# Kernel tuning notes

Measured on AMD Instinct MI355X. Metric: run time of the kernel, lower is better.

Reference implementation:

```python
import jax, jax.numpy as jnp
import numpy as np

B, S, D, H, E, K = 2, 1024, 768, 12, 8, 2
DF = 4 * D
HD = D // H
EPS = 1e-5

def layer_norm(x, g, b):
    m = jnp.mean(x, axis=-1, keepdims=True)
    v = jnp.mean(jnp.square(x - m), axis=-1, keepdims=True)
    return (x - m) * jax.lax.rsqrt(v + EPS) * g + b

def setup_inputs() -> dict:
    key = jax.random.key(0)
    ks = jax.random.split(key, 16)
    s = lambda i, shape, sc: jax.random.normal(ks[i], shape, jnp.float32) * sc
    return {
        'x': s(0, (B, S, D), 1.0),
        'ln1_g': jnp.ones((D,), jnp.float32), 'ln1_b': jnp.zeros((D,), jnp.float32),
        'Wq': s(1, (D, D), 0.02), 'Wk': s(2, (D, D), 0.02), 'Wv': s(3, (D, D), 0.02),
        'Wo': s(4, (D, D), 0.02), 'bo': jnp.zeros((D,), jnp.float32),
        'ln2_g': jnp.ones((D,), jnp.float32), 'ln2_b': jnp.zeros((D,), jnp.float32),
        'Wr': s(5, (D, E), 0.02), 'br': jnp.zeros((E,), jnp.float32),
        'W1': s(6, (E, D, DF), 0.02), 'b1': jnp.zeros((E, DF), jnp.float32),
        'W2': s(7, (E, DF, D), 0.02), 'b2': jnp.zeros((E, D), jnp.float32),
    }

def _attn(xn, Wq, Wk, Wv, Wo, bo):
    # xn: [B,S,D]
    q = (xn @ Wq).reshape(B, S, H, HD).transpose(0, 2, 1, 3)
    k = (xn @ Wk).reshape(B, S, H, HD).transpose(0, 2, 1, 3)
    v = (xn @ Wv).reshape(B, S, H, HD).transpose(0, 2, 1, 3)
    scores = jnp.einsum('bhqd,bhkd->bhqk', q, k) / jnp.sqrt(jnp.float32(HD))
    causal = jnp.tril(jnp.ones((S, S), bool))
    scores = jnp.where(causal, scores, jnp.float32(-1e9))
    w = jax.nn.softmax(scores, axis=-1)
    out = jnp.einsum('bhqk,bhkd->bhqd', w, v)
    out = out.transpose(0, 2, 1, 3).reshape(B, S, D)
    return out @ Wo + bo

def _smoe(xn, Wr, br, W1, b1, W2, b2):
    logits = xn @ Wr + br                               # [B,S,E]
    topv, topi = jax.lax.top_k(logits, K)               # [B,S,K]
    gw = jax.nn.softmax(topv, axis=-1)                  # softmax over selected experts
    oh = jax.nn.one_hot(topi, E, dtype=xn.dtype)        # [B,S,K,E]
    gate = jnp.einsum('bske,bsk->bse', oh, gw)          # sparse gate, zeros elsewhere
    h = jax.nn.gelu(jnp.einsum('bsd,edf->bsef', xn, W1) + b1, approximate=False)
    eo = jnp.einsum('bsef,efd->bsed', h, W2) + b2       # [B,S,E,D]
    return jnp.einsum('bsed,bse->bsd', eo, gate)

def reference(x, ln1_g, ln1_b, Wq, Wk, Wv, Wo, bo, ln2_g, ln2_b, Wr, br, W1, b1, W2, b2):
    h = x + _attn(layer_norm(x, ln1_g, ln1_b), Wq, Wk, Wv, Wo, bo)
    out = h + _smoe(layer_norm(h, ln2_g, ln2_b), Wr, br, W1, b1, W2, b2)
    return out
```

## Files before the change

kernel.cpp:

```cpp
#include <hip/hip_runtime.h>

using bf16x8 = __attribute__((ext_vector_type(8))) short;
using f32x4  = __attribute__((ext_vector_type(4))) float;

#define DEV __device__ __forceinline__

DEV short f2bf(float x){
  unsigned u = __float_as_uint(x);
  u += 0x7fffu + ((u >> 16) & 1u);
  return (short)(u >> 16);
}
DEV float bf2f(short h){ return __uint_as_float(((unsigned)(unsigned short)h) << 16); }

#define MFMA16(a,b,c) __builtin_amdgcn_mfma_f32_16x16x32_bf16(a,b,c,0,0,0)

DEV void gl_lds16(const void* g, void* l){
  __builtin_amdgcn_global_load_lds(
      (const __attribute__((address_space(1))) unsigned*)g,
      (__attribute__((address_space(3))) unsigned*)l, 16, 0, 0);
}


__global__ void k_transpose(const float* __restrict__ src, long sbatch,
                            short* __restrict__ dhi, short* __restrict__ dlo, long dbatch,
                            int R, int C){
  __shared__ float tile[64][65];
  const float* s = src + (long)blockIdx.z * sbatch;
  int c0 = blockIdx.x * 64, r0 = blockIdx.y * 64;
  int tx = threadIdx.x & 15, ty = threadIdx.x >> 4;
  #pragma unroll
  for (int i = 0; i < 4; i++){
    int r = ty + 16*i;
    float4 v = *(const float4*)&s[(long)(r0 + r) * C + c0 + tx*4];
    tile[r][tx*4+0] = v.x; tile[r][tx*4+1] = v.y;
    tile[r][tx*4+2] = v.z; tile[r][tx*4+3] = v.w;
  }
  __syncthreads();
  int rseg = (threadIdx.x & 7) * 8;
  #pragma unroll
  for (int p = 0; p < 2; p++){
    int col = (threadIdx.x >> 3) + 32*p;
    short hv[8], lv[8];
    #pragma unroll
    for (int k = 0; k < 8; k++){
      float v = tile[rseg + k][col];
      hv[k] = f2bf(v);
      lv[k] = f2bf(v - bf2f(hv[k]));
    }
    long o = (long)blockIdx.z * dbatch + (long)(c0 + col) * R + r0 + rseg;
    *(bf16x8*)&dhi[o] = *(bf16x8*)&hv[0];
    if (dlo) *(bf16x8*)&dlo[o] = *(bf16x8*)&lv[0];
  }
}

__global__ void k_ln1(const float* __restrict__ x, const float* __restrict__ g,
                      const float* __restrict__ bb,
                      short* __restrict__ xh, short* __restrict__ xl){
  int t = blockIdx.x, tid = threadIdx.x;
  const float* xr = x + (long)t * 768;
  float v[3];
  #pragma unroll
  for (int j = 0; j < 3; j++) v[j] = xr[tid + 256*j];
  float s = v[0]+v[1]+v[2];
  float q = v[0]*v[0]+v[1]*v[1]+v[2]*v[2];
  #pragma unroll
  for (int o = 32; o > 0; o >>= 1){ s += __shfl_down(s,o,64); q += __shfl_down(q,o,64); }
  __shared__ float ss[4], qs[4];
  int w = tid >> 6;
  if ((tid & 63) == 0){ ss[w] = s; qs[w] = q; }
  __syncthreads();
  float St = ss[0]+ss[1]+ss[2]+ss[3], Qt = qs[0]+qs[1]+qs[2]+qs[3];
  float mean = St * (1.f/768.f);
  float var  = Qt * (1.f/768.f) - mean*mean;
  float inv  = 1.f / sqrtf(var + 1e-5f);
  #pragma unroll
  for (int j = 0; j < 3; j++){
    int d = tid + 256*j;
    float xn = (v[j]-mean)*inv*g[d] + bb[d];
    short hv = f2bf(xn);
    xh[(long)t*768 + d] = hv;
    xl[(long)t*768 + d] = f2bf(xn - bf2f(hv));
  }
}

__global__ __launch_bounds__(256,2) void k_qkv(
    const short* __restrict__ Ah, const short* __restrict__ Al,
    const short* __restrict__ Bh, const short* __restrict__ Bl,
    short* __restrict__ qh, short* __restrict__ ql,
    short* __restrict__ kh, short* __restrict__ kl,
    short* __restrict__ vh, short* __restrict__ vl){
  int M0 = blockIdx.x * 128, N0 = blockIdx.y * 128;
  __shared__ __align__(16) short lah[128*64], lal[128*64], lbh[128*64], lbl[128*64];
  int tid = threadIdx.x;
  int w = tid >> 6, lane = tid & 63, l15 = lane & 15, quad = lane >> 4;
  int mbase = (w & 1) * 64, nbase = (w >> 1) * 64;
  f32x4 acc[4][4];
  #pragma unroll
  for (int i = 0; i < 4; i++)
    #pragma unroll
    for (int j = 0; j < 4; j++) acc[i][j] = (f32x4){0.f,0.f,0.f,0.f};
  int rl = lane >> 3, pch = lane & 7;
  long gA[4], gB[4];
  #pragma unroll
  for (int j = 0; j < 4; j++){
    int r = w*32 + j*8 + rl;
    int c = pch ^ (r & 7);
    gA[j] = (long)(M0 + r)*768 + c*8;
    gB[j] = (long)(N0 + r)*768 + c*8;
  }
  for (int k0 = 0; k0 < 768; k0 += 64){
    #pragma unroll
    for (int j = 0; j < 4; j++){
      gl_lds16(Ah + gA[j] + k0, lah + w*2048 + j*512);
      gl_lds16(Al + gA[j] + k0, lal + w*2048 + j*512);
      gl_lds16(Bh + gB[j] + k0, lbh + w*2048 + j*512);
      gl_lds16(Bl + gB[j] + k0, lbl + w*2048 + j*512);
    }
    __syncthreads();
    #pragma unroll
    for (int kk = 0; kk < 2; kk++){
      int swq = ((kk*4 + quad) ^ (l15 & 7)) * 8;
      bf16x8 afh[4], afl[4];
      #pragma unroll
      for (int mt = 0; mt < 4; mt++){
        afh[mt] = *(const bf16x8*)&lah[(mbase+mt*16+l15)*64 + swq];
        afl[mt] = *(const bf16x8*)&lal[(mbase+mt*16+l15)*64 + swq];
      }
      #pragma unroll
      for (int nt = 0; nt < 4; nt++){
        bf16x8 bfh = *(const bf16x8*)&lbh[(nbase+nt*16+l15)*64 + swq];
        bf16x8 bfl = *(const bf16x8*)&lbl[(nbase+nt*16+l15)*64 + swq];
        #pragma unroll
        for (int mt = 0; mt < 4; mt++){
          acc[mt][nt] = MFMA16(afh[mt], bfh, acc[mt][nt]);
          acc[mt][nt] = MFMA16(afh[mt], bfl, acc[mt][nt]);
          acc[mt][nt] = MFMA16(afl[mt], bfh, acc[mt][nt]);
        }
      }
    }
    __syncthreads();
  }
  #pragma unroll
  for (int mt = 0; mt < 4; mt++){
    #pragma unroll
    for (int nt = 0; nt < 4; nt++){
      #pragma unroll
      for (int rg = 0; rg < 4; rg++){
        int m = M0 + mbase + mt*16 + quad*4 + rg;
        int n = N0 + nbase + nt*16 + l15;
        float vv = acc[mt][nt][rg];
        int bi = m >> 10, si = m & 1023;
        if (n < 768){
          float sv = vv * 0.125f;
          short hv = f2bf(sv);
          int hh = n >> 6, hd = n & 63;
          long o = (((long)(bi*12+hh)*1024) + si)*64 + hd;
          qh[o] = hv; ql[o] = f2bf(sv - bf2f(hv));
        } else if (n < 1536){
          int n2 = n - 768;
          short hv = f2bf(vv);
          int hh = n2 >> 6, hd = n2 & 63;
          long o = (((long)(bi*12+hh)*1024) + si)*64 + hd;
          kh[o] = hv; kl[o] = f2bf(vv - bf2f(hv));
        } else {
          int n2 = n - 1536;
          short hv = f2bf(vv);
          int hh = n2 >> 6, hd = n2 & 63;
          long o = (((long)(bi*12+hh)*64) + hd)*1024 + si;
          vh[o] = hv; vl[o] = f2bf(vv - bf2f(hv));
        }
      }
    }
  }
}

__global__ __launch_bounds__(256,3) void k_attn(
    const short* __restrict__ qh, const short* __restrict__ ql,
    const short* __restrict__ kh, const short* __restrict__ kl,
    const short* __restrict__ vth, const short* __restrict__ vtl,
    float* __restrict__ po, float* __restrict__ pm, float* __restrict__ pl){
  int qt = blockIdx.x >> 1, half = blockIdx.x & 1, bh = blockIdx.y;
  int q0 = qt * 64;
  long base = (long)bh * 1024 * 64;
  int ktb = half ? ((qt + 2) >> 1) : 0;
  int kte = half ? (qt + 1) : ((qt + 2) >> 1);
  __shared__ __align__(16) short skh[64*64], skl[64*64], svh[64*64], svl[64*64];
  __shared__ __align__(16) short sph[4][16*72], spl[4][16*72];
  int tid = threadIdx.x, w = tid >> 6, lane = tid & 63, l15 = lane & 15, quad = lane >> 4;
  bf16x8 qfh[2], qfl[2];
  #pragma unroll
  for (int c = 0; c < 2; c++){
    long qa = base + (long)(q0 + w*16 + l15)*64 + c*32 + quad*8;
    qfh[c] = *(const bf16x8*)(qh + qa);
    qfl[c] = *(const bf16x8*)(ql + qa);
  }
  f32x4 oacc[4];
  #pragma unroll
  for (int i = 0; i < 4; i++) oacc[i] = (f32x4){0.f,0.f,0.f,0.f};
  float m_i[4] = {-1e30f,-1e30f,-1e30f,-1e30f};
  float l_i[4] = {0.f,0.f,0.f,0.f};
  const short* gsrc = (w==0) ? kh : (w==1) ? kl : (w==2) ? vth : vtl;
  short* myb = (w==0) ? skh : (w==1) ? skl : (w==2) ? svh : svl;
  bool isv = (w >= 2);
  int rloc = lane >> 3, pch = lane & 7;
  for (int kt = ktb; kt < kte; kt++){
    #pragma unroll
    for (int j = 0; j < 8; j++){
      int r = j*8 + rloc;
      int c = pch ^ (r & 7);
      long ga = isv ? (base + (long)r*1024 + kt*64 + c*8)
                    : (base + (long)(kt*64 + r)*64 + c*8);
      gl_lds16(gsrc + ga, myb + j*512);
    }
    __syncthreads();
    f32x4 sfr[4];
    #pragma unroll
    for (int nt = 0; nt < 4; nt++){
      f32x4 c = (f32x4){0.f,0.f,0.f,0.f};
      int krow = (nt*16 + l15) * 64;
      #pragma unroll
      for (int ch = 0; ch < 2; ch++){
        int pc = ((ch*4 + quad) ^ (l15 & 7)) * 8;
        bf16x8 kfh = *(const bf16x8*)&skh[krow + pc];
        bf16x8 kfl = *(const bf16x8*)&skl[krow + pc];
        c = MFMA16(qfh[ch], kfh, c);
        c = MFMA16(qfh[ch], kfl, c);
        c = MFMA16(qfl[ch], kfh, c);
      }
      sfr[nt] = c;
    }
    if (kt == qt){
      #pragma unroll
      for (int nt = 0; nt < 4; nt++)
        #pragma unroll
        for (int rg = 0; rg < 4; rg++){
          int kp = nt*16 + l15, qp = w*16 + quad*4 + rg;
          if (kp > qp) sfr[nt][rg] = -1e30f;
        }
    }
    float rmax[4];
    #pragma unroll
    for (int rg = 0; rg < 4; rg++)
      rmax[rg] = fmaxf(fmaxf(sfr[0][rg], sfr[1][rg]), fmaxf(sfr[2][rg], sfr[3][rg]));
    #pragma unroll
    for (int xm = 1; xm < 16; xm <<= 1)
      #pragma unroll
      for (int rg = 0; rg < 4; rg++)
        rmax[rg] = fmaxf(rmax[rg], __shfl_xor(rmax[rg], xm, 64));
    float alpha[4];
    #pragma unroll
    for (int rg = 0; rg < 4; rg++){
      float mn = fmaxf(m_i[rg], rmax[rg]);
      alpha[rg] = expf(m_i[rg] - mn);
      m_i[rg] = mn;
    }
    float rsum[4] = {0.f,0.f,0.f,0.f};
    #pragma unroll
    for (int nt = 0; nt < 4; nt++)
      #pragma unroll
      for (int rg = 0; rg < 4; rg++){
        float p = expf(sfr[nt][rg] - m_i[rg]);
        sfr[nt][rg] = p; rsum[rg] += p;
      }
    #pragma unroll
    for (int xm = 1; xm < 16; xm <<= 1)
      #pragma unroll
      for (int rg = 0; rg < 4; rg++)
        rsum[rg] += __shfl_xor(rsum[rg], xm, 64);
    #pragma unroll
    for (int rg = 0; rg < 4; rg++) l_i[rg] = l_i[rg]*alpha[rg] + rsum[rg];
    #pragma unroll
    for (int hd = 0; hd < 4; hd++)
      #pragma unroll
      for (int rg = 0; rg < 4; rg++) oacc[hd][rg] *= alpha[rg];
    #pragma unroll
    for (int nt = 0; nt < 4; nt++)
      #pragma unroll
      for (int rg = 0; rg < 4; rg++){
        float p = sfr[nt][rg];
        short hv = f2bf(p);
        sph[w][(quad*4+rg)*72 + nt*16 + l15] = hv;
        spl[w][(quad*4+rg)*72 + nt*16 + l15] = f2bf(p - bf2f(hv));
      }
    bf16x8 pfh[2], pfl[2];
    #pragma unroll
    for (int ch = 0; ch < 2; ch++){
      pfh[ch] = *(const bf16x8*)&sph[w][l15*72 + ch*32 + quad*8];
      pfl[ch] = *(const bf16x8*)&spl[w][l15*72 + ch*32 + quad*8];
    }
    #pragma unroll
    for (int hd = 0; hd < 4; hd++){
      int vrow = (hd*16 + l15) * 64;
      #pragma unroll
      for (int ch = 0; ch < 2; ch++){
        int pc = ((ch*4 + quad) ^ (l15 & 7)) * 8;
        bf16x8 vfh = *(const bf16x8*)&svh[vrow + pc];
        bf16x8 vfl = *(const bf16x8*)&svl[vrow + pc];
        oacc[hd] = MFMA16(pfh[ch], vfh, oacc[hd]);
        oacc[hd] = MFMA16(pfh[ch], vfl, oacc[hd]);
        oacc[hd] = MFMA16(pfl[ch], vfh, oacc[hd]);
      }
    }
    __syncthreads();
  }
  long pb = ((long)(half*24 + bh)*1024);
  #pragma unroll
  for (int hdt = 0; hdt < 4; hdt++)
    #pragma unroll
    for (int rg = 0; rg < 4; rg++){
      int qp = q0 + w*16 + quad*4 + rg;
      po[(pb + qp)*64 + hdt*16 + l15] = oacc[hdt][rg];
    }
  if (l15 == 0){
    #pragma unroll
    for (int rg = 0; rg < 4; rg++){
      int qp = q0 + w*16 + quad*4 + rg;
      pm[pb + qp] = m_i[rg];
      pl[pb + qp] = l_i[rg];
    }
  }
}

__global__ void k_attn_combine(const float* __restrict__ po, const float* __restrict__ pm,
                               const float* __restrict__ pl,
                               short* __restrict__ oh, short* __restrict__ ol){
  int bh = blockIdx.y, tid = threadIdx.x;
  int r = blockIdx.x*64 + (tid >> 2);
  int c0 = (tid & 3) * 16;
  long i0 = (long)bh*1024 + r;
  long i1 = (long)(24 + bh)*1024 + r;
  float m0 = pm[i0], m1 = pm[i1], l0 = pl[i0], l1 = pl[i1];
  float m = fmaxf(m0, m1);
  float a0 = expf(m0 - m), a1 = expf(m1 - m);
  float inv = 1.f / (a0*l0 + a1*l1);
  a0 *= inv; a1 *= inv;
  int b = bh / 12, hh = bh % 12;
  long ob = ((long)(b*1024 + r))*768 + hh*64 + c0;
  short hv[16], lv[16];
  #pragma unroll
  for (int j = 0; j < 4; j++){
    float4 o0 = *(const float4*)&po[i0*64 + c0 + j*4];
    float4 o1 = *(const float4*)&po[i1*64 + c0 + j*4];
    float vs[4] = {a0*o0.x + a1*o1.x, a0*o0.y + a1*o1.y,
                   a0*o0.z + a1*o1.z, a0*o0.w + a1*o1.w};
    #pragma unroll
    for (int q = 0; q < 4; q++){
      short h = f2bf(vs[q]);
      hv[j*4+q] = h; lv[j*4+q] = f2bf(vs[q] - bf2f(h));
    }
  }
  *(bf16x8*)(oh + ob)     = *(bf16x8*)&hv[0];
  *(bf16x8*)(oh + ob + 8) = *(bf16x8*)&hv[8];
  *(bf16x8*)(ol + ob)     = *(bf16x8*)&lv[0];
  *(bf16x8*)(ol + ob + 8) = *(bf16x8*)&lv[8];
}

__global__ __launch_bounds__(256,2) void k_wo(
    const short* __restrict__ Ah, const short* __restrict__ Al,
    const short* __restrict__ Bh, const short* __restrict__ Bl,
    const float* __restrict__ x, const float* __restrict__ bo,
    float* __restrict__ hout){
  int M0 = blockIdx.x * 128, N0 = blockIdx.y * 128;
  __shared__ __align__(16) short lah[128*64], lal[128*64], lbh[128*64], lbl[128*64];
  int tid = threadIdx.x;
  int w = tid >> 6, lane = tid & 63, l15 = lane & 15, quad = lane >> 4;
  int mbase = (w & 1) * 64, nbase = (w >> 1) * 64;
  f32x4 acc[4][4];
  #pragma unroll
  for (int i = 0; i < 4; i++)
    #pragma unroll
    for (int j = 0; j < 4; j++) acc[i][j] = (f32x4){0.f,0.f,0.f,0.f};
  int rl = lane >> 3, pch = lane & 7;
  long gA[4], gB[4];
  #pragma unroll
  for (int j = 0; j < 4; j++){
    int r = w*32 + j*8 + rl;
    int c = pch ^ (r & 7);
    gA[j] = (long)(M0 + r)*768 + c*8;
    gB[j] = (long)(N0 + r)*768 + c*8;
  }
  for (int k0 = 0; k0 < 768; k0 += 64){
    #pragma unroll
    for (int j = 0; j < 4; j++){
      gl_lds16(Ah + gA[j] + k0, lah + w*2048 + j*512);
      gl_lds16(Al + gA[j] + k0, lal + w*2048 + j*512);
      gl_lds16(Bh + gB[j] + k0, lbh + w*2048 + j*512);
      gl_lds16(Bl + gB[j] + k0, lbl + w*2048 + j*512);
    }
    __syncthreads();
    #pragma unroll
    for (int kk = 0; kk < 2; kk++){
      int swq = ((kk*4 + quad) ^ (l15 & 7)) * 8;
      bf16x8 afh[4], afl[4];
      #pragma unroll
      for (int mt = 0; mt < 4; mt++){
        afh[mt] = *(const bf16x8*)&lah[(mbase+mt*16+l15)*64 + swq];
        afl[mt] = *(const bf16x8*)&lal[(mbase+mt*16+l15)*64 + swq];
      }
      #pragma unroll
      for (int nt = 0; nt < 4; nt++){
        bf16x8 bfh = *(const bf16x8*)&lbh[(nbase+nt*16+l15)*64 + swq];
        bf16x8 bfl = *(const bf16x8*)&lbl[(nbase+nt*16+l15)*64 + swq];
        #pragma unroll
        for (int mt = 0; mt < 4; mt++){
          acc[mt][nt] = MFMA16(afh[mt], bfh, acc[mt][nt]);
          acc[mt][nt] = MFMA16(afh[mt], bfl, acc[mt][nt]);
          acc[mt][nt] = MFMA16(afl[mt], bfh, acc[mt][nt]);
        }
      }
    }
    __syncthreads();
  }
  #pragma unroll
  for (int mt = 0; mt < 4; mt++)
    #pragma unroll
    for (int nt = 0; nt < 4; nt++)
      #pragma unroll
      for (int rg = 0; rg < 4; rg++){
        int m = M0 + mbase + mt*16 + quad*4 + rg;
        int n = N0 + nbase + nt*16 + l15;
        hout[(long)m*768 + n] = acc[mt][nt][rg] + x[(long)m*768 + n] + bo[n];
      }
}

__global__ void k_ln2router(const float* __restrict__ h, const float* __restrict__ g,
                            const float* __restrict__ bb, const float* __restrict__ Wr,
                            const float* __restrict__ br, short* __restrict__ xn2,
                            int* __restrict__ sel, float* __restrict__ gw){
  int wv = (blockIdx.x*256 + threadIdx.x) >> 6;
  int lane = threadIdx.x & 63;
  #pragma unroll
  for (int rep = 0; rep < 2; rep++){
    int t = wv*2 + rep;
    const float* xr = h + (long)t * 768;
    float v[12];
    #pragma unroll
    for (int j = 0; j < 12; j++) v[j] = xr[lane + 64*j];
    float s = 0.f, q = 0.f;
    #pragma unroll
    for (int j = 0; j < 12; j++){ s += v[j]; q += v[j]*v[j]; }
    #pragma unroll
    for (int xm = 1; xm < 64; xm <<= 1){ s += __shfl_xor(s, xm, 64); q += __shfl_xor(q, xm, 64); }
    float mean = s * (1.f/768.f);
    float var  = q * (1.f/768.f) - mean*mean;
    float inv  = 1.f / sqrtf(var + 1e-5f);
    float part[8] = {0,0,0,0,0,0,0,0};
    #pragma unroll
    for (int j = 0; j < 12; j++){
      int d = lane + 64*j;
      float xn = (v[j]-mean)*inv*g[d] + bb[d];
      xn2[(long)t*768 + d] = f2bf(xn);
      #pragma unroll
      for (int e = 0; e < 8; e++) part[e] += xn * Wr[d*8 + e];
    }
    #pragma unroll
    for (int xm = 1; xm < 64; xm <<= 1)
      #pragma unroll
      for (int e = 0; e < 8; e++) part[e] += __shfl_xor(part[e], xm, 64);
    if (lane == 0){
      float lg[8];
      #pragma unroll
      for (int e = 0; e < 8; e++) lg[e] = part[e] + br[e];
      int i1 = 0;
      for (int e = 1; e < 8; e++) if (lg[e] > lg[i1]) i1 = e;
      int i2 = -1;
      for (int e = 0; e < 8; e++){ if (e == i1) continue; if (i2 < 0 || lg[e] > lg[i2]) i2 = e; }
      float e2 = expf(lg[i2] - lg[i1]);
      float is = 1.f / (1.f + e2);
      gw[t*2]   = is;
      gw[t*2+1] = e2 * is;
      sel[t*2]   = i1;
      sel[t*2+1] = i2;
    }
  }
}

__global__ void k_build(const int* __restrict__ sel, int* __restrict__ poffs,
                        int* __restrict__ mbc, int* __restrict__ ptot,
                        int* __restrict__ pperm, int* __restrict__ inv){
  __shared__ int cnt8[8], cur[8], wbase[16][8];
  int tid = threadIdx.x;
  int lane = tid & 63, wv = tid >> 6;
  if (tid < 8) cnt8[tid] = 0;
  __syncthreads();
  int sv[4];
  #pragma unroll
  for (int r = 0; r < 4; r++){
    sv[r] = sel[tid + r*1024];
    #pragma unroll
    for (int e = 0; e < 8; e++){
      unsigned long long mk = __ballot(sv[r] == e);
      if (lane == 0) atomicAdd(&cnt8[e], (int)__popcll(mk));
    }
  }
  __syncthreads();
  if (tid == 0){
    int p = 0;
    for (int e = 0; e < 8; e++){
      cur[e] = p; poffs[e] = p;
      int pc = (cnt8[e] + 127) & ~127;
      mbc[e] = pc >> 7;
      p += pc;
    }
    *ptot = p;
  }
  __syncthreads();
  #pragma unroll
  for (int r = 0; r < 5; r++) pperm[tid + r*1024] = -1;
  __syncthreads();
  unsigned long long lmask = (1ull << lane) - 1ull;
  #pragma unroll
  for (int r = 0; r < 4; r++){
    int s = sv[r];
    unsigned long long mk[8];
    #pragma unroll
    for (int e = 0; e < 8; e++) mk[e] = __ballot(s == e);
    if (lane == 0){
      #pragma unroll
      for (int e = 0; e < 8; e++)
        wbase[wv][e] = atomicAdd(&cur[e], (int)__popcll(mk[e]));
    }
    unsigned long long mks = 0;
    #pragma unroll
    for (int e = 0; e < 8; e++) if (s == e) mks = mk[e];
    int pos = wbase[wv][s] + (int)__popcll(mks & lmask);
    int i = tid + r*1024;
    pperm[pos] = i;
    inv[i] = pos;
  }
}

__global__ __launch_bounds__(256,3) void k_moe1(
    const short* __restrict__ xn2, const short* __restrict__ W1T,
    const float* __restrict__ b1,
    const int* __restrict__ poffs, const int* __restrict__ mbc,
    const int* __restrict__ pperm, short* __restrict__ h1){
  int t = blockIdx.x;
  int e = t / 24, n = t % 24;
  if ((int)blockIdx.y >= mbc[e]) return;
  int M0 = poffs[e] + blockIdx.y * 128;
  int N0 = n * 128;
  const short* Bp = W1T + (long)e * 3072 * 768;
  __shared__ __align__(16) short la[128*64], lb[128*64];
  __shared__ int rtok[128];
  int tid = threadIdx.x, w = tid >> 6, lane = tid & 63, l15 = lane & 15, quad = lane >> 4;
  if (tid < 128) rtok[tid] = pperm[M0 + tid];
  __syncthreads();
  int rl = lane >> 3, pch = lane & 7;
  long gA[4], gB[4];
  #pragma unroll
  for (int j = 0; j < 4; j++){
    int r = w*32 + j*8 + rl;
    int c = pch ^ (r & 7);
    int tk = rtok[r]; tk = (tk >= 0) ? (tk >> 1) : 0;
    gA[j] = (long)tk*768 + c*8;
    gB[j] = (long)(N0 + r)*768 + c*8;
  }
  short* ldA = la + w*2048;
  short* ldB = lb + w*2048;
  f32x4 acc[4][4];
  #pragma unroll
  for (int i = 0; i < 4; i++)
    #pragma unroll
    for (int j = 0; j < 4; j++) acc[i][j] = (f32x4){0.f,0.f,0.f,0.f};
  int mbase = (w & 1) * 64, nbase = (w >> 1) * 64;
  for (int k0 = 0; k0 < 768; k0 += 64){
    #pragma unroll
    for (int j = 0; j < 4; j++) gl_lds16(xn2 + gA[j] + k0, ldA + j*512);
    #pragma unroll
    for (int j = 0; j < 4; j++) gl_lds16(Bp  + gB[j] + k0, ldB + j*512);
    __syncthreads();
    #pragma unroll
    for (int kk = 0; kk < 2; kk++){
      int swq = ((kk*4 + quad) ^ (l15 & 7)) * 8;
      bf16x8 af[4];
      #pragma unroll
      for (int mt = 0; mt < 4; mt++)
        af[mt] = *(const bf16x8*)&la[(mbase+mt*16+l15)*64 + swq];
      #pragma unroll
      for (int nt = 0; nt < 4; nt++){
        bf16x8 bf = *(const bf16x8*)&lb[(nbase+nt*16+l15)*64 + swq];
        #pragma unroll
        for (int mt = 0; mt < 4; mt++) acc[mt][nt] = MFMA16(af[mt], bf, acc[mt][nt]);
      }
    }
    __syncthreads();
  }
  #pragma unroll
  for (int mt = 0; mt < 4; mt++)
    #pragma unroll
    for (int nt = 0; nt < 4; nt++)
      #pragma unroll
      for (int rg = 0; rg < 4; rg++){
        int ml = mbase + mt*16 + quad*4 + rg;
        if (rtok[ml] >= 0){
          int nn = N0 + nbase + nt*16 + l15;
          float vv = acc[mt][nt][rg] + b1[e*3072 + nn];
          float gl = 0.5f * vv * (1.f + erff(vv * 0.70710678118654752f));
          h1[(long)(M0 + ml)*3072 + nn] = f2bf(gl);
        }
      }
}

__global__ __launch_bounds__(256,4) void k_moe2(
    const short* __restrict__ h1, const short* __restrict__ W2T,
    const float* __restrict__ b2,
    const int* __restrict__ poffs, const int* __restrict__ mbc,
    float* __restrict__ e0, float* __restrict__ e1,
    float* __restrict__ e2, float* __restrict__ e3){
  int t = blockIdx.x;
  int e = t / 24, r24 = t % 24;
  int n = r24 >> 2, ks = r24 & 3;
  if ((int)blockIdx.y >= mbc[e]) return;
  int M0 = poffs[e] + blockIdx.y * 128;
  int N0 = n * 128;
  int kbeg = ks * 768;
  const short* Bp = W2T + (long)e * 768 * 3072;
  float* eo = (ks == 0) ? e0 : (ks == 1) ? e1 : (ks == 2) ? e2 : e3;
  __shared__ __align__(16) short la[128*64], lb[128*64];
  int tid = threadIdx.x, w = tid >> 6, lane = tid & 63, l15 = lane & 15, quad = lane >> 4;
  int rl = lane >> 3, pch = lane & 7;
  long gA[4], gB[4];
  #pragma unroll
  for (int j = 0; j < 4; j++){
    int r = w*32 + j*8 + rl;
    int c = pch ^ (r & 7);
    gA[j] = (long)(M0 + r)*3072 + kbeg + c*8;
    gB[j] = (long)(N0 + r)*3072 + kbeg + c*8;
  }
  short* ldA = la + w*2048;
  short* ldB = lb + w*2048;
  f32x4 acc[4][4];
  #pragma unroll
  for (int i = 0; i < 4; i++)
    #pragma unroll
    for (int j = 0; j < 4; j++) acc[i][j] = (f32x4){0.f,0.f,0.f,0.f};
  int mbase = (w & 1) * 64, nbase = (w >> 1) * 64;
  for (int k0 = 0; k0 < 768; k0 += 64){
    #pragma unroll
    for (int j = 0; j < 4; j++) gl_lds16(h1 + gA[j] + k0, ldA + j*512);
    #pragma unroll
    for (int j = 0; j < 4; j++) gl_lds16(Bp + gB[j] + k0, ldB + j*512);
    __syncthreads();
    #pragma unroll
    for (int kk = 0; kk < 2; kk++){
      int swq = ((kk*4 + quad) ^ (l15 & 7)) * 8;
      bf16x8 af[4];
      #pragma unroll
      for (int mt = 0; mt < 4; mt++)
        af[mt] = *(const bf16x8*)&la[(mbase+mt*16+l15)*64 + swq];
      #pragma unroll
      for (int nt = 0; nt < 4; nt++){
        bf16x8 bf = *(const bf16x8*)&lb[(nbase+nt*16+l15)*64 + swq];
        #pragma unroll
        for (int mt = 0; mt < 4; mt++) acc[mt][nt] = MFMA16(af[mt], bf, acc[mt][nt]);
      }
    }
    __syncthreads();
  }
  #pragma unroll
  for (int mt = 0; mt < 4; mt++)
    #pragma unroll
    for (int nt = 0; nt < 4; nt++)
      #pragma unroll
      for (int rg = 0; rg < 4; rg++){
        int ml = mbase + mt*16 + quad*4 + rg;
        int nn = N0 + nbase + nt*16 + l15;
        float vv = acc[mt][nt][rg] + ((ks == 0) ? b2[e*768 + nn] : 0.f);
        eo[(long)(M0 + ml)*768 + nn] = vv;
      }
}

__global__ void k_combine(const float* __restrict__ h,
                          const float* __restrict__ e0, const float* __restrict__ e1,
                          const float* __restrict__ e2, const float* __restrict__ e3,
                          const int* __restrict__ inv, const float* __restrict__ gw,
                          float* __restrict__ out){
  int i = blockIdx.x * 256 + threadIdx.x;
  int t = i / 192, c = i - t * 192;
  int s0 = inv[2*t], s1 = inv[2*t+1];
  float g0 = gw[2*t], g1 = gw[2*t+1];
  float4 a  = ((const float4*)h)[i];
  long o0 = (long)s0*192 + c, o1 = (long)s1*192 + c;
  float4 x0 = ((const float4*)e0)[o0];
  float4 y0 = ((const float4*)e1)[o0];
  float4 z0 = ((const float4*)e2)[o0];
  float4 w0 = ((const float4*)e3)[o0];
  float4 x1 = ((const float4*)e0)[o1];
  float4 y1 = ((const float4*)e1)[o1];
  float4 z1 = ((const float4*)e2)[o1];
  float4 w1 = ((const float4*)e3)[o1];
  float4 o;
  o.x = a.x + g0*(x0.x + y0.x + z0.x + w0.x) + g1*(x1.x + y1.x + z1.x + w1.x);
  o.y = a.y + g0*(x0.y + y0.y + z0.y + w0.y) + g1*(x1.y + y1.y + z1.y + w1.y);
  o.z = a.z + g0*(x0.z + y0.z + z0.z + w0.z) + g1*(x1.z + y1.z + z1.z + w1.z);
  o.w = a.w + g0*(x0.w + y0.w + z0.w + w0.w) + g1*(x1.w + y1.w + z1.w + w1.w);
  ((float4*)out)[i] = o;
}

extern "C" void kernel_launch(void* const* d_in, const int* in_sizes, int n_in,
                              void* d_out, int out_size, void* d_ws, size_t ws_size,
                              hipStream_t stream){
  const float* x    = (const float*)d_in[0];
  const float* ln1g = (const float*)d_in[1];
  const float* ln1b = (const float*)d_in[2];
  const float* Wq   = (const float*)d_in[3];
  const float* Wk   = (const float*)d_in[4];
  const float* Wv   = (const float*)d_in[5];
  const float* Wo   = (const float*)d_in[6];
  const float* bo   = (const float*)d_in[7];
  const float* ln2g = (const float*)d_in[8];
  const float* ln2b = (const float*)d_in[9];
  const float* Wr   = (const float*)d_in[10];
  const float* br   = (const float*)d_in[11];
  const float* W1   = (const float*)d_in[12];
  const float* b1   = (const float*)d_in[13];
  const float* W2   = (const float*)d_in[14];
  const float* b2   = (const float*)d_in[15];

  char* ws = (char*)d_ws;
  size_t off = 0;
  auto alloc = [&](size_t bytes) -> void* {
    void* p = ws + off;
    off += (bytes + 255) & ~(size_t)255;
    return p;
  };
  short* WQKVH = (short*)alloc(2304l*768*2);
  short* WQKVL = (short*)alloc(2304l*768*2);
  short* WOH   = (short*)alloc(768l*768*2);
  short* WOL   = (short*)alloc(768l*768*2);
  short* W1T   = (short*)alloc(8l*3072*768*2);
  short* W2T   = (short*)alloc(8l*768*3072*2);
  short* XN1H  = (short*)alloc(2048l*768*2);
  short* XN1L  = (short*)alloc(2048l*768*2);
  short* QH    = (short*)alloc(2048l*768*2);
  short* QL    = (short*)alloc(2048l*768*2);
  short* KH    = (short*)alloc(2048l*768*2);
  short* KL    = (short*)alloc(2048l*768*2);
  short* VTH   = (short*)alloc(2048l*768*2);
  short* VTL   = (short*)alloc(2048l*768*2);
  short* ATH   = (short*)alloc(2048l*768*2);
  short* ATL   = (short*)alloc(2048l*768*2);
  float* HBUF  = (float*)alloc(2048l*768*4);
  short* XN2   = (short*)alloc(2048l*768*2);
  short* H1    = (short*)alloc(5120l*3072*2);
  float* E0    = (float*)alloc(5120l*768*4);
  float* E1    = (float*)alloc(5120l*768*4);
  float* PO    = (float*)alloc(2l*24*1024*64*4);
  float* PM    = (float*)alloc(2l*24*1024*4);
  float* PL    = (float*)alloc(2l*24*1024*4);
  int*   POFF  = (int*)alloc(8*4);
  int*   MBC   = (int*)alloc(8*4);
  int*   PTOT  = (int*)alloc(4);
  int*   SEL   = (int*)alloc(4096*4);
  int*   PPERM = (int*)alloc(5120*4);
  int*   INV   = (int*)alloc(4096*4);
  float* GW    = (float*)alloc(4096*4);
  (void)ws_size; (void)in_sizes; (void)n_in; (void)out_size;

  float* E2 = (float*)XN1H;
  float* E3 = E2 + 5120l*768;

  k_transpose<<<dim3(12,12,1),256,0,stream>>>(Wq, 0, WQKVH,             WQKVL,             0, 768, 768);
  k_transpose<<<dim3(12,12,1),256,0,stream>>>(Wk, 0, WQKVH + 768l*768,  WQKVL + 768l*768,  0, 768, 768);
  k_transpose<<<dim3(12,12,1),256,0,stream>>>(Wv, 0, WQKVH + 1536l*768, WQKVL + 1536l*768, 0, 768, 768);
  k_transpose<<<dim3(12,12,1),256,0,stream>>>(Wo, 0, WOH, WOL, 0, 768, 768);
  k_transpose<<<dim3(48,12,8),256,0,stream>>>(W1, 768l*3072, W1T, nullptr, 3072l*768, 768, 3072);
  k_transpose<<<dim3(12,48,8),256,0,stream>>>(W2, 3072l*768, W2T, nullptr, 768l*3072, 3072, 768);

  k_ln1<<<2048,256,0,stream>>>(x, ln1g, ln1b, XN1H, XN1L);
  k_qkv<<<dim3(16,18),256,0,stream>>>(XN1H, XN1L, WQKVH, WQKVL, QH, QL, KH, KL, VTH, VTL);
  k_attn<<<dim3(32,24),256,0,stream>>>(QH, QL, KH, KL, VTH, VTL, PO, PM, PL);
  k_attn_combine<<<dim3(16,24),256,0,stream>>>(PO, PM, PL, ATH, ATL);
  k_wo<<<dim3(16,6),256,0,stream>>>(ATH, ATL, WOH, WOL, x, bo, HBUF);

  k_ln2router<<<256,256,0,stream>>>(HBUF, ln2g, ln2b, Wr, br, XN2, SEL, GW);
  k_build<<<1,1024,0,stream>>>(SEL, POFF, MBC, PTOT, PPERM, INV);
  k_moe1<<<dim3(192,16),256,0,stream>>>(XN2, W1T, b1, POFF, MBC, PPERM, H1);
  k_moe2<<<dim3(192,16),256,0,stream>>>(H1, W2T, b2, POFF, MBC, E0, E1, E2, E3);
  k_combine<<<1536,256,0,stream>>>(HBUF, E0, E1, E2, E3, INV, GW, (float*)d_out);
}
```

Measured before the change: 467.7 us.

## Shrink QKV/Wo GEMM M-tiles to 64 and split-K the Wo projection

```diff
diff --git a/kernel.cpp b/kernel.cpp
--- a/kernel.cpp
+++ b/kernel.cpp
@@ -83,36 +83,44 @@
   }
 }
 
-__global__ __launch_bounds__(256,2) void k_qkv(
+__global__ __launch_bounds__(256,3) void k_qkv(
     const short* __restrict__ Ah, const short* __restrict__ Al,
     const short* __restrict__ Bh, const short* __restrict__ Bl,
     short* __restrict__ qh, short* __restrict__ ql,
     short* __restrict__ kh, short* __restrict__ kl,
     short* __restrict__ vh, short* __restrict__ vl){
-  int M0 = blockIdx.x * 128, N0 = blockIdx.y * 128;
-  __shared__ __align__(16) short lah[128*64], lal[128*64], lbh[128*64], lbl[128*64];
+  int M0 = blockIdx.x * 64, N0 = blockIdx.y * 128;
+  __shared__ __align__(16) short lah[64*64], lal[64*64], lbh[128*64], lbl[128*64];
   int tid = threadIdx.x;
   int w = tid >> 6, lane = tid & 63, l15 = lane & 15, quad = lane >> 4;
-  int mbase = (w & 1) * 64, nbase = (w >> 1) * 64;
-  f32x4 acc[4][4];
-  #pragma unroll
-  for (int i = 0; i < 4; i++)
+  int mbase = (w & 1) * 32, nbase = (w >> 1) * 64;
+  f32x4 acc[2][4];
+  #pragma unroll
+  for (int i = 0; i < 2; i++)
     #pragma unroll
     for (int j = 0; j < 4; j++) acc[i][j] = (f32x4){0.f,0.f,0.f,0.f};
   int rl = lane >> 3, pch = lane & 7;
-  long gA[4], gB[4];
+  long gA[2], gB[4];
+  #pragma unroll
+  for (int j = 0; j < 2; j++){
+    int r = w*16 + j*8 + rl;
+    int c = pch ^ (r & 7);
+    gA[j] = (long)(M0 + r)*768 + c*8;
+  }
   #pragma unroll
   for (int j = 0; j < 4; j++){
     int r = w*32 + j*8 + rl;
     int c = pch ^ (r & 7);
-    gA[j] = (long)(M0 + r)*768 + c*8;
     gB[j] = (long)(N0 + r)*768 + c*8;
   }
   for (int k0 = 0; k0 < 768; k0 += 64){
     #pragma unroll
+    for (int j = 0; j < 2; j++){
+      gl_lds16(Ah + gA[j] + k0, lah + w*1024 + j*512);
+      gl_lds16(Al + gA[j] + k0, lal + w*1024 + j*512);
+    }
+    #pragma unroll
     for (int j = 0; j < 4; j++){
-      gl_lds16(Ah + gA[j] + k0, lah + w*2048 + j*512);
-      gl_lds16(Al + gA[j] + k0, lal + w*2048 + j*512);
       gl_lds16(Bh + gB[j] + k0, lbh + w*2048 + j*512);
       gl_lds16(Bl + gB[j] + k0, lbl + w*2048 + j*512);
     }
@@ -120,9 +128,9 @@
     #pragma unroll
     for (int kk = 0; kk < 2; kk++){
       int swq = ((kk*4 + quad) ^ (l15 & 7)) * 8;
-      bf16x8 afh[4], afl[4];
-      #pragma unroll
-      for (int mt = 0; mt < 4; mt++){
+      bf16x8 afh[2], afl[2];
+      #pragma unroll
+      for (int mt = 0; mt < 2; mt++){
         afh[mt] = *(const bf16x8*)&lah[(mbase+mt*16+l15)*64 + swq];
         afl[mt] = *(const bf16x8*)&lal[(mbase+mt*16+l15)*64 + swq];
       }
@@ -131,7 +139,7 @@
         bf16x8 bfh = *(const bf16x8*)&lbh[(nbase+nt*16+l15)*64 + swq];
         bf16x8 bfl = *(const bf16x8*)&lbl[(nbase+nt*16+l15)*64 + swq];
         #pragma unroll
-        for (int mt = 0; mt < 4; mt++){
+        for (int mt = 0; mt < 2; mt++){
           acc[mt][nt] = MFMA16(afh[mt], bfh, acc[mt][nt]);
           acc[mt][nt] = MFMA16(afh[mt], bfl, acc[mt][nt]);
           acc[mt][nt] = MFMA16(afl[mt], bfh, acc[mt][nt]);
@@ -141,7 +149,7 @@
     __syncthreads();
   }
   #pragma unroll
-  for (int mt = 0; mt < 4; mt++){
+  for (int mt = 0; mt < 2; mt++){
     #pragma unroll
     for (int nt = 0; nt < 4; nt++){
       #pragma unroll
@@ -355,35 +363,45 @@
   *(bf16x8*)(ol + ob + 8) = *(bf16x8*)&lv[8];
 }
 
-__global__ __launch_bounds__(256,2) void k_wo(
+__global__ __launch_bounds__(256,3) void k_wo(
     const short* __restrict__ Ah, const short* __restrict__ Al,
     const short* __restrict__ Bh, const short* __restrict__ Bl,
-    const float* __restrict__ x, const float* __restrict__ bo,
-    float* __restrict__ hout){
-  int M0 = blockIdx.x * 128, N0 = blockIdx.y * 128;
-  __shared__ __align__(16) short lah[128*64], lal[128*64], lbh[128*64], lbl[128*64];
+    float* __restrict__ p0, float* __restrict__ p1){
+  int M0 = blockIdx.x * 64, N0 = blockIdx.y * 128;
+  int ks = blockIdx.z;
+  int kbeg = ks * 384;
+  float* wp = ks ? p1 : p0;
+  __shared__ __align__(16) short lah[64*64], lal[64*64], lbh[128*64], lbl[128*64];
   int tid = threadIdx.x;
   int w = tid >> 6, lane = tid & 63, l15 = lane & 15, quad = lane >> 4;
-  int mbase = (w & 1) * 64, nbase = (w >> 1) * 64;
-  f32x4 acc[4][4];
-  #pragma unroll
-  for (int i = 0; i < 4; i++)
+  int mbase = (w & 1) * 32, nbase = (w >> 1) * 64;
+  f32x4 acc[2][4];
+  #pragma unroll
+  for (int i = 0; i < 2; i++)
     #pragma unroll
     for (int j = 0; j < 4; j++) acc[i][j] = (f32x4){0.f,0.f,0.f,0.f};
   int rl = lane >> 3, pch = lane & 7;
-  long gA[4], gB[4];
+  long gA[2], gB[4];
+  #pragma unroll
+  for (int j = 0; j < 2; j++){
+    int r = w*16 + j*8 + rl;
+    int c = pch ^ (r & 7);
+    gA[j] = (long)(M0 + r)*768 + kbeg + c*8;
+  }
   #pragma unroll
   for (int j = 0; j < 4; j++){
     int r = w*32 + j*8 + rl;
     int c = pch ^ (r & 7);
-    gA[j] = (long)(M0 + r)*768 + c*8;
-    gB[j] = (long)(N0 + r)*768 + c*8;
-  }
-  for (int k0 = 0; k0 < 768; k0 += 64){
+    gB[j] = (long)(N0 + r)*768 + kbeg + c*8;
+  }
+  for (int k0 = 0; k0 < 384; k0 += 64){
+    #pragma unroll
+    for (int j = 0; j < 2; j++){
+      gl_lds16(Ah + gA[j] + k0, lah + w*1024 + j*512);
+      gl_lds16(Al + gA[j] + k0, lal + w*1024 + j*512);
+    }
     #pragma unroll
     for (int j = 0; j < 4; j++){
-      gl_lds16(Ah + gA[j] + k0, lah + w*2048 + j*512);
-      gl_lds16(Al + gA[j] + k0, lal + w*2048 + j*512);
       gl_lds16(Bh + gB[j] + k0, lbh + w*2048 + j*512);
       gl_lds16(Bl + gB[j] + k0, lbl + w*2048 + j*512);
     }
@@ -391,9 +409,9 @@
     #pragma unroll
     for (int kk = 0; kk < 2; kk++){
       int swq = ((kk*4 + quad) ^ (l15 & 7)) * 8;
-      bf16x8 afh[4], afl[4];
-      #pragma unroll
-      for (int mt = 0; mt < 4; mt++){
+      bf16x8 afh[2], afl[2];
+      #pragma unroll
+      for (int mt = 0; mt < 2; mt++){
         afh[mt] = *(const bf16x8*)&lah[(mbase+mt*16+l15)*64 + swq];
         afl[mt] = *(const bf16x8*)&lal[(mbase+mt*16+l15)*64 + swq];
       }
@@ -402,7 +420,7 @@
         bf16x8 bfh = *(const bf16x8*)&lbh[(nbase+nt*16+l15)*64 + swq];
         bf16x8 bfl = *(const bf16x8*)&lbl[(nbase+nt*16+l15)*64 + swq];
         #pragma unroll
-        for (int mt = 0; mt < 4; mt++){
+        for (int mt = 0; mt < 2; mt++){
           acc[mt][nt] = MFMA16(afh[mt], bfh, acc[mt][nt]);
           acc[mt][nt] = MFMA16(afh[mt], bfl, acc[mt][nt]);
           acc[mt][nt] = MFMA16(afl[mt], bfh, acc[mt][nt]);
@@ -412,15 +430,32 @@
     __syncthreads();
   }
   #pragma unroll
-  for (int mt = 0; mt < 4; mt++)
+  for (int mt = 0; mt < 2; mt++)
     #pragma unroll
     for (int nt = 0; nt < 4; nt++)
       #pragma unroll
       for (int rg = 0; rg < 4; rg++){
         int m = M0 + mbase + mt*16 + quad*4 + rg;
         int n = N0 + nbase + nt*16 + l15;
-        hout[(long)m*768 + n] = acc[mt][nt][rg] + x[(long)m*768 + n] + bo[n];
-      }
+        wp[(long)m*768 + n] = acc[mt][nt][rg];
+      }
+}
+
+__global__ void k_wo_combine(const float* __restrict__ p0, const float* __restrict__ p1,
+                             const float* __restrict__ x, const float* __restrict__ bo,
+                             float* __restrict__ hout){
+  int i = blockIdx.x * 256 + threadIdx.x;
+  int c = i % 192;
+  float4 a = ((const float4*)p0)[i];
+  float4 b = ((const float4*)p1)[i];
+  float4 xx = ((const float4*)x)[i];
+  float4 bb = ((const float4*)bo)[c];
+  float4 o;
+  o.x = a.x + b.x + xx.x + bb.x;
+  o.y = a.y + b.y + xx.y + bb.y;
+  o.z = a.z + b.z + xx.z + bb.z;
+  o.w = a.w + b.w + xx.w + bb.w;
+  ((float4*)hout)[i] = o;
 }
 
 __global__ void k_ln2router(const float* __restrict__ h, const float* __restrict__ g,
@@ -760,6 +795,8 @@
 
   float* E2 = (float*)XN1H;
   float* E3 = E2 + 5120l*768;
+  float* WP0 = PO;
+  float* WP1 = PO + 2048l*768;
 
   k_transpose<<<dim3(12,12,1),256,0,stream>>>(Wq, 0, WQKVH,             WQKVL,             0, 768, 768);
   k_transpose<<<dim3(12,12,1),256,0,stream>>>(Wk, 0, WQKVH + 768l*768,  WQKVL + 768l*768,  0, 768, 768);
@@ -769,10 +806,11 @@
   k_transpose<<<dim3(12,48,8),256,0,stream>>>(W2, 3072l*768, W2T, nullptr, 768l*3072, 3072, 768);
 
   k_ln1<<<2048,256,0,stream>>>(x, ln1g, ln1b, XN1H, XN1L);
-  k_qkv<<<dim3(16,18),256,0,stream>>>(XN1H, XN1L, WQKVH, WQKVL, QH, QL, KH, KL, VTH, VTL);
+  k_qkv<<<dim3(32,18),256,0,stream>>>(XN1H, XN1L, WQKVH, WQKVL, QH, QL, KH, KL, VTH, VTL);
   k_attn<<<dim3(32,24),256,0,stream>>>(QH, QL, KH, KL, VTH, VTL, PO, PM, PL);
   k_attn_combine<<<dim3(16,24),256,0,stream>>>(PO, PM, PL, ATH, ATL);
-  k_wo<<<dim3(16,6),256,0,stream>>>(ATH, ATL, WOH, WOL, x, bo, HBUF);
+  k_wo<<<dim3(32,6,2),256,0,stream>>>(ATH, ATL, WOH, WOL, WP0, WP1);
+  k_wo_combine<<<1536,256,0,stream>>>(WP0, WP1, x, bo, HBUF);
 
   k_ln2router<<<256,256,0,stream>>>(HBUF, ln2g, ln2b, Wr, br, XN2, SEL, GW);
   k_build<<<1,1024,0,stream>>>(SEL, POFF, MBC, PTOT, PPERM, INV);
```

After: 447.8 us. 4.3% less time.
